# Kernel optimization log

Measured on AMD Instinct MI355X. Metric: run time of the kernel, lower is better.

The kernel has to match this reference:

```python
import jax, jax.numpy as jnp
import numpy as np

B = 30          # bandwidth
L = B           # degrees l = 0..L-1
NB = 2 * B      # spatial grid size per angle (beta/alpha/gamma)
MW = 2 * L - 1  # centered frequency index width, m in [-(L-1), L-1]
P = 6           # kernel grid points (n_alpha=6, n_beta=1)


def _wigner_d_all(betas, L):
    """Wigner-d matrices d^l_{m,n}(beta) via d^l(beta)=expm(-(beta/2)(J+ - J-)).
    Returns [len(betas), L, MW, MW], zero-padded for |m|,|n|>l."""
    betas = np.asarray(betas, dtype=np.float64)
    D = np.zeros((len(betas), L, MW, MW), dtype=np.float64)
    for l in range(L):
        dim = 2 * l + 1
        m = np.arange(-l, l)
        cp = np.sqrt(l * (l + 1) - m * (m + 1))  # <m+1|J+|m>
        A = np.zeros((dim, dim))
        A[np.arange(1, dim), np.arange(dim - 1)] = cp
        A = A - A.T  # J+ - J-, real antisymmetric
        lam, V = np.linalg.eigh(1j * A)  # Hermitian
        ph = np.exp(0.5j * betas[:, None] * lam[None, :])  # [nb, dim]
        dl = np.einsum('ab,jb,cb->jac', V, ph, V.conj()).real
        off = L - 1 - l
        D[:, l, off:off + dim, off:off + dim] = dl
    return D


def _s3_quadrature(b):
    """SOFT-grid quadrature weights over beta (lie_learn S3 formula, up to a constant)."""
    j = np.arange(2 * b)
    k = np.arange(b)[None, :]
    s = (np.sin(np.pi * (2 * j[:, None] + 1) * (2 * k + 1) / (4 * b)) / (2 * k + 1)).sum(axis=1)
    return (2.0 / b) * np.sin(np.pi * (2 * j + 1) / (4 * b)) * s


# ---- precomputed constants ----
_betas_sig = np.pi * (2 * np.arange(NB) + 1) / (4 * B)  # SOFT beta grid
_D_np = _wigner_d_all(_betas_sig, L)                    # [NB, L, MW, MW]
_alphas_k = np.linspace(0.0, 2.0 * np.pi, P, endpoint=False)
_Dk_np = _wigner_d_all(np.full(P, np.pi / 160.0), L)[:, :, :, L - 1]  # [P, L, MW], n=0 column
_idx_c = (np.arange(MW) - (L - 1)) % NB                 # centered m -> FFT bin
_nidx = np.arange(MW) - (L - 1)

D_SIG = jnp.asarray(_D_np, dtype=jnp.float32)
D0_SIG = jnp.asarray(_D_np[:, :, :, L - 1], dtype=jnp.float32)
D_KER = jnp.asarray(_Dk_np, dtype=jnp.float32)
W_QUAD = jnp.asarray(_s3_quadrature(B), dtype=jnp.float32)
FAC_L = jnp.asarray(2 * np.arange(L) + 1, dtype=jnp.float32)
E_KER = jnp.asarray(np.exp(-1j * _nidx[None, :] * _alphas_k[:, None]), dtype=jnp.complex64)


def s2_conv(x, wk):
    """FFT-based S2 convolution: S2 analysis -> spectral multiply -> SO(3) synthesis.
    x: [batch, f_in, NB(beta), NB(alpha)] real; wk: [f_in, f_out, P].
    Returns [batch, f_out, NB(beta), NB(alpha), NB(gamma)] real."""
    xf = jnp.fft.fft(x, axis=-1) * (2.0 * np.pi / NB)        # alpha -> m, complex64
    xfc = xf[..., _idx_c]                                     # centered m: [b,f,NB,MW]
    # S2 analysis: X^l_m = sum_beta w(beta) d^l_{m0}(beta) xhat(beta, m)
    X = jnp.einsum('j,jlm,bfjm->bflm', W_QUAD, D0_SIG, xfc)   # [b,f_in,L,MW]
    # kernel spectrum psi^l_n = sum_p wk_p d^l_{n0}(beta_p) e^{-i n alpha_p}
    psi = jnp.einsum('iop,pln,pn->ioln', wk.astype(jnp.complex64),
                     D_KER.astype(jnp.complex64), E_KER)      # [f_in,f_out,L,MW]
    # spectral mm: Z^l_{mn} = sum_{f_in} X^l_m conj(psi^l_n)
    Z = jnp.einsum('bilm,ioln->bolmn', X, jnp.conj(psi))      # [b,f_out,L,MW,MW]
    # SO(3) synthesis per beta: F(beta,m,n) = sum_l (2l+1) d^l_{mn}(beta) Z^l_{mn}
    F = jnp.einsum('l,jlmn,bolmn->bojmn', FAC_L, D_SIG, Z)    # [b,f_out,NB,MW,MW]
    G = jnp.zeros(F.shape[:3] + (NB, NB), dtype=F.dtype)
    G = G.at[..., _idx_c[:, None], _idx_c[None, :]].set(F)    # embed centered freqs
    return jnp.fft.ifft2(G, axes=(-2, -1)).real * float(NB * NB)


def so3_integrate_gamma(x):
    # matches the given so3_integrate: contracts ONLY the last (gamma) axis with w
    return jnp.einsum('...g,g->...', x, W_QUAD)


def setup_inputs() -> dict:
    key = jax.random.key(0)
    k1, k2, k3 = jax.random.split(key, 3)
    batch = 16
    x1 = jax.random.normal(k1, (batch, 2, NB, NB), dtype=jnp.float32)
    w_conv = jax.random.normal(k2, (2, 10, P), dtype=jnp.float32) / np.sqrt(2 * P)
    w_deconv = jax.random.normal(k3, (10, 2, P), dtype=jnp.float32) / np.sqrt(10 * P)
    return {"x1": x1, "w_conv": w_conv, "w_deconv": w_deconv}


def reference(x1, w_conv, w_deconv):
    x = s2_conv(x1, w_conv)        # encode: [b,10,60,60,60]
    x = so3_integrate_gamma(x)     # [b,10,60,60] (S2 signal)
    x = s2_conv(x, w_deconv)       # decode: [b,2,60,60,60]
    return so3_integrate_gamma(x)  # [b,2,60,60]
```

## Files before the change

kernel.cpp:

```cpp
#include <hip/hip_runtime.h>
#include <hip/hip_fp16.h>

#define NBG   60
#define LMAX  30
#define MWC   59
#define CTR   29
#define NPAIR 20
#define NT    11
#define NTP   12
#define NOFF  5
#define PI_F  3.14159265358979323846f

__device__ void wigner_colf(float beta, int mp, int mn, float scale,
                            float* out, int stride) {
  int a = mp - mn; if (a < 0) a = -a;
  int b = mp + mn; if (b < 0) b = -b;
  int lmin = (a + b) >> 1;
  for (int l = 0; l < LMAX; ++l) out[l * stride] = 0.0f;
  if (lmin >= LMAX) return;
  float sh, ch; sincosf(0.5f * beta, &sh, &ch);
  float x = ch * ch - sh * sh;
  float base = scale;
  for (int q = 0; q < a; ++q) base *= sh;
  for (int q = 0; q < b; ++q) base *= ch;
  if (mp >= mn && ((mp - mn) & 1)) base = -base;
  float K2 = 1.f;
  for (int q = 1; q <= a; ++q) K2 *= (float)(b + q) / (float)q;
  float Pm2 = 0.f, Pm1 = 1.f;
  out[lmin * stride] = base * sqrtf(K2);
  for (int s = 1; lmin + s < LMAX; ++s) {
    float Ps;
    if (s == 1) {
      Ps = (a + 1) + (a + b + 2) * 0.5f * (x - 1.f);
    } else {
      float t0 = 2.f * s + a + b;
      float c1 = 2.f * s * (s + a + b) * (t0 - 2.f);
      float c2 = (t0 - 1.f) * (t0 * (t0 - 2.f) * x + (float)(a * a - b * b));
      float c3 = 2.f * (s + a - 1.f) * (s + b - 1.f) * t0;
      Ps = (c2 * Pm1 - c3 * Pm2) / c1;
    }
    K2 *= ((float)s * (s + a + b)) / (((float)s + a) * ((float)s + b));
    out[(lmin + s) * stride] = base * sqrtf(K2) * Ps;
    Pm2 = Pm1; Pm1 = Ps;
  }
}

__device__ __forceinline__ float quad_w(int j) {
  float s = 0.f;
  for (int k = 0; k < 30; ++k) {
    int r = ((2 * j + 1) * (2 * k + 1)) % 240;
    s += sinf(2.f * PI_F * r / 240.f) / (float)(2 * k + 1);
  }
  return (2.f / 30.f) * sinf(PI_F * (2 * j + 1) / 120.f) * s;
}

__global__ __launch_bounds__(256)
void k1_prep(const float* __restrict__ x1,
             const float* __restrict__ wc, const float* __restrict__ wd,
             float2* __restrict__ scwF1, float2* __restrict__ scwF2,
             float* __restrict__ D0T, float* __restrict__ sgd,
             float2* __restrict__ xfT) {
  __shared__ __align__(16) char smem[13056];
  int u = blockIdx.x, t = threadIdx.x;
  if (u == 0) {
    float*  swq  = (float*)smem;
    float2* swqn = (float2*)(smem + 256);
    if (t < NBG) swq[t] = quad_w(t);
    __syncthreads();
    if (t < NT) {
      int n = t - NOFF;
      float re = 0.f, im = 0.f;
      for (int g = 0; g < NBG; ++g) {
        int k = ((n * g) % NBG + NBG) % NBG;
        float sn, cs; sincosf(2.f * PI_F * k / 60.f, &sn, &cs);
        re += swq[g] * cs; im += swq[g] * sn;
      }
      swqn[t] = make_float2(re, im);
    }
    __syncthreads();
    if (t < NT * NPAIR) {
      int nn = t / NPAIR, pair = t - nn * NPAIR, n = nn - NOFF;
      float re1 = 0, im1 = 0, re2 = 0, im2 = 0;
      for (int p = 0; p < 6; ++p) {
        int k = ((n * p) % 6 + 6) % 6;
        float sn, cs; sincosf(2.f * PI_F * k / 6.f, &sn, &cs);
        float a1 = wc[pair * 6 + p], a2 = wd[pair * 6 + p];
        re1 += a1 * cs; im1 += a1 * sn;
        re2 += a2 * cs; im2 += a2 * sn;
      }
      float2 w = swqn[nn];
      scwF1[t] = make_float2(w.x * re1 - w.y * im1, w.x * im1 + w.y * re1);
      scwF2[t] = make_float2(PI_F * (w.x * re2 - w.y * im2),
                             PI_F * (w.x * im2 + w.y * re2));
    }
  } else if (u < 60) {
    int M = u - 1;
    if (t < NBG) {
      float wqj = quad_w(t);
      wigner_colf(PI_F * (2 * t + 1) / 120.f, M - CTR, 0, wqj,
                  D0T + (size_t)M * LMAX * NBG + t, NBG);
    }
  } else if (u < 300) {
    float* buf  = (float*)smem;
    float* dkwL = (float*)(smem + 11520);
    int s = u - 60, j = s >> 2, c = s & 3;
    int M0 = c * 8, nM = (c < 3) ? 8 : 6;
    if (t < nM * NT) {
      int Mi = t / NT, nn = t - Mi * NT;
      wigner_colf(PI_F * (2 * j + 1) / 120.f, M0 + Mi - CTR, nn - NOFF, 1.f,
                  &buf[Mi * 360 + nn], NTP);
    } else if (t >= 128 && t < 128 + NT) {
      int nn = t - 128;
      wigner_colf(PI_F / 160.f, nn - NOFF, 0, 1.f, dkwL + nn, NTP);
      for (int l = 0; l < LMAX; ++l) dkwL[l * NTP + nn] *= (float)(2 * l + 1);
    }
    __syncthreads();
    size_t base = (size_t)(j * 30 + M0) * 360;
    for (int q = t; q < nM * 360; q += 256) {
      int r = q % 360, nn = r % NTP;
      sgd[base + q] = (nn < NT) ? buf[q] * dkwL[r] : 0.f;
    }
  } else {
    float*  xr  = (float*)smem;
    float*  twc = (float*)(smem + 1920);
    float*  tws = (float*)(smem + 2160);
    float2* xo  = (float2*)(smem + 2400);
    int s = u - 300, j = s >> 2, qh = s & 3;
    for (int q = t; q < 8 * NBG; q += 256) {
      int bl = q / NBG, a = q - bl * NBG;
      xr[bl * NBG + a] = x1[((size_t)(qh * 8 + bl) * NBG + j) * NBG + a];
    }
    if (t < NBG) {
      float sn, cs; sincosf(-2.f * PI_F * t / 60.f, &sn, &cs);
      twc[t] = cs; tws[t] = sn;
    }
    __syncthreads();
    for (int q = t; q < 8 * MWC; q += 256) {
      int bl = q / MWC, M = q - bl * MWC, mm = M - CTR;
      const float* xp = xr + bl * NBG;
      float re = 0.f, im = 0.f; int k = 0;
      for (int a = 0; a < NBG; ++a) {
        re += xp[a] * twc[k]; im += xp[a] * tws[k];
        k += mm; if (k >= NBG) k -= NBG; if (k < 0) k += NBG;
      }
      const float sc = 2.f * PI_F / 60.f;
      xo[M * 9 + bl] = make_float2(re * sc, im * sc);
    }
    __syncthreads();
    for (int q = t; q < MWC * 8; q += 256) {
      int M = q / 8, bl = q - M * 8;
      xfT[((size_t)M * NBG + j) * 32 + qh * 8 + bl] = xo[M * 9 + bl];
    }
  }
}

__global__ __launch_bounds__(256)
void k_ana1(const float2* __restrict__ xfT, const float* __restrict__ D0T,
            float2* __restrict__ X21) {
  __shared__ float2 sxf[NBG][16];
  __shared__ float  sD[8][NBG];
  int bi = blockIdx.x;
  int M = bi >> 3, lq = (bi >> 1) & 3, wh = bi & 1;
  int t = threadIdx.x;
  for (int q = t; q < NBG * 16; q += 256) {
    int jj = q >> 4, b = q & 15;
    sxf[jj][b] = xfT[((size_t)M * NBG + jj) * 32 + b * 2 + wh];
  }
  for (int q = t; q < 8 * NBG; q += 256) {
    int ll = q / NBG, jj = q - ll * NBG, l = lq * 8 + ll;
    sD[ll][jj] = (l < LMAX) ? D0T[((size_t)M * LMAX + l) * NBG + jj] : 0.f;
  }
  __syncthreads();
  if (t < 128) {
    int ll = t >> 4, b = t & 15;
    int l = lq * 8 + ll;
    if (l < LMAX) {
      float re = 0.f, im = 0.f;
#pragma unroll 6
      for (int jj = 0; jj < NBG; ++jj) {
        float d = sD[ll][jj];
        float2 v = sxf[jj][b];
        re += d * v.x; im += d * v.y;
      }
      X21[(size_t)M * LMAX * 32 + l * 32 + wh * 16 + b] = make_float2(re, im);
    }
  }
}

__global__ __launch_bounds__(256)
void k_core1(const float2* __restrict__ X2, const float* __restrict__ sgd,
             const float2* __restrict__ scwF, __half2* __restrict__ Th) {
  __shared__ float  sg[2][LMAX][NTP];
  __shared__ float2 scw[NT * NPAIR];
  __shared__ float2 sC[2][LMAX][NPAIR];
  int t = threadIdx.x;
  int j = blockIdx.x / 30, mg = blockIdx.x - 30 * j;
  int Mbase = mg * 2;
  for (int q = t; q < NT * NPAIR; q += 256) scw[q] = scwF[q];
  for (int q = t; q < 2 * LMAX * NTP; q += 256) {
    int Mi = q / (LMAX * NTP), r = q - Mi * LMAX * NTP;
    int l = r / NTP, nn = r - l * NTP;
    int M = Mbase + Mi;
    float v = 0.f;
    if (M < MWC && nn < NT) {
      if (M < 30) {
        v = sgd[(size_t)(j * 30 + M) * 360 + r];
      } else {
        v = sgd[(size_t)(j * 30 + 58 - M) * 360 + l * NTP + (10 - nn)];
        if (!(M & 1)) v = -v;
      }
    }
    ((float*)sg)[q] = v;
  }
  __syncthreads();
  for (int q = t; q < 2 * LMAX * NPAIR; q += 256) {
    int Mi = q / (LMAX * NPAIR), r = q - Mi * LMAX * NPAIR;
    int l = r / NPAIR, pair = r - l * NPAIR;
    float cre = 0.f, cim = 0.f;
#pragma unroll
    for (int nn = 0; nn < NT; ++nn) {
      float g = sg[Mi][l][nn];
      float2 c = scw[nn * NPAIR + pair];
      cre += g * c.x; cim += g * c.y;
    }
    ((float2*)sC)[q] = make_float2(cre, cim);
  }
  __syncthreads();
  for (int q = t; q < 2 * 160; q += 256) {
    int Mi = q / 160, u = q - Mi * 160;
    int M = Mbase + Mi;
    if (M >= MWC) continue;
    int bb = u / 10, o = u - 10 * bb;
    float tre = 0.f, tim = 0.f;
#pragma unroll 6
    for (int l = 0; l < LMAX; ++l) {
#pragma unroll
      for (int i = 0; i < 2; ++i) {
        float2 xv = X2[((size_t)M * LMAX + l) * 32 + i * 16 + bb];
        float2 cv = sC[Mi][l][i * 10 + o];
        tre += xv.x * cv.x - xv.y * cv.y;
        tim += xv.x * cv.y + xv.y * cv.x;
      }
    }
    Th[((size_t)j * MWC + M) * 160 + u] = __floats2half2_rn(tre, tim);
  }
}

__global__ __launch_bounds__(256)
void k_ana2(const __half2* __restrict__ T1, const float* __restrict__ D0T,
            float2* __restrict__ X22) {
  __shared__ float2 sxf[NBG][10];
  __shared__ float  sD[LMAX][NBG];
  int M = blockIdx.x >> 4, c = blockIdx.x & 15;
  int u0 = c * 10, t = threadIdx.x;
  for (int q = t; q < NBG * 10; q += 256) {
    int jj = q / 10, w = q - jj * 10;
    float2 v1 = __half22float2(T1[((size_t)jj * MWC + M) * 160 + u0 + w]);
    float2 v2 = __half22float2(T1[((size_t)jj * MWC + (58 - M)) * 160 + u0 + w]);
    sxf[jj][w] = make_float2(v1.x + v2.x, v1.y - v2.y);
  }
  for (int q = t; q < LMAX * NBG; q += 256) ((float*)sD)[q] = D0T[(size_t)M * LMAX * NBG + q];
  __syncthreads();
  for (int q = t; q < LMAX * 10; q += 256) {
    int l = q / 10, w = q - l * 10;
    float re = 0.f, im = 0.f;
#pragma unroll 6
    for (int jj = 0; jj < NBG; ++jj) {
      float d = sD[l][jj];
      float2 v = sxf[jj][w];
      re += d * v.x; im += d * v.y;
    }
    X22[((size_t)M * LMAX + l) * 160 + w * 16 + c] = make_float2(re, im);
  }
}

__global__ __launch_bounds__(256)
void k_core2(const float2* __restrict__ X2, const float* __restrict__ sgd,
             const float2* __restrict__ scwF, float2* __restrict__ Tf) {
  __shared__ float  sg[2][LMAX][NTP];
  __shared__ float2 scw[NT * NPAIR];
  __shared__ float2 sC[2][LMAX][NPAIR];
  __shared__ float2 sRed[256];
  int t = threadIdx.x;
  int j = blockIdx.x / 30, mg = blockIdx.x - 30 * j;
  int Mbase = mg * 2;
  for (int q = t; q < NT * NPAIR; q += 256) scw[q] = scwF[q];
  for (int q = t; q < 2 * LMAX * NTP; q += 256) {
    int Mi = q / (LMAX * NTP), r = q - Mi * LMAX * NTP;
    int l = r / NTP, nn = r - l * NTP;
    int M = Mbase + Mi;
    float v = 0.f;
    if (M < MWC && nn < NT) {
      if (M < 30) {
        v = sgd[(size_t)(j * 30 + M) * 360 + r];
      } else {
        v = sgd[(size_t)(j * 30 + 58 - M) * 360 + l * NTP + (10 - nn)];
        if (!(M & 1)) v = -v;
      }
    }
    ((float*)sg)[q] = v;
  }
  __syncthreads();
  for (int q = t; q < 2 * LMAX * NPAIR; q += 256) {
    int Mi = q / (LMAX * NPAIR), r = q - Mi * LMAX * NPAIR;
    int l = r / NPAIR, pair = r - l * NPAIR;
    float cre = 0.f, cim = 0.f;
#pragma unroll
    for (int nn = 0; nn < NT; ++nn) {
      float g = sg[Mi][l][nn];
      float2 c = scw[nn * NPAIR + pair];
      cre += g * c.x; cim += g * c.y;
    }
    ((float2*)sC)[q] = make_float2(cre, cim);
  }
  __syncthreads();
  int sub = t >> 6, idx = t & 63;
  int Mi = idx >> 5, u = idx & 31;
  int M = Mbase + Mi;
  int bb = u >> 1, o = u & 1;
  float tre = 0.f, tim = 0.f;
  if (M < MWC) {
    for (int l = sub; l < LMAX; l += 4) {
#pragma unroll
      for (int i = 0; i < 10; ++i) {
        float2 xv = X2[((size_t)M * LMAX + l) * 160 + i * 16 + bb];
        float2 cv = sC[Mi][l][i * 2 + o];
        tre += xv.x * cv.x - xv.y * cv.y;
        tim += xv.x * cv.y + xv.y * cv.x;
      }
    }
  }
  sRed[t] = make_float2(tre, tim);
  __syncthreads();
  if (t < 64 && M < MWC) {
    float2 a0 = sRed[t], a1 = sRed[t + 64], a2 = sRed[t + 128], a3 = sRed[t + 192];
    Tf[((size_t)j * MWC + M) * 32 + u] =
        make_float2(a0.x + a1.x + a2.x + a3.x, a0.y + a1.y + a2.y + a3.y);
  }
}

__global__ __launch_bounds__(256)
void k_synth2(const float2* __restrict__ T2, float* __restrict__ out) {
  __shared__ float2 sT[MWC][8];
  __shared__ float twc[NBG], tws[NBG];
  int j = blockIdx.x >> 2, uq = blockIdx.x & 3;
  int u0 = uq * 8, t = threadIdx.x;
  for (int q = t; q < MWC * 8; q += 256) {
    int M = q >> 3, uu = q & 7;
    sT[M][uu] = T2[((size_t)j * MWC + M) * 32 + u0 + uu];
  }
  if (t < NBG) {
    float s, c; sincosf(2.f * PI_F * t / 60.f, &s, &c);
    twc[t] = c; tws[t] = s;
  }
  __syncthreads();
  for (int q = t; q < 8 * NBG; q += 256) {
    int uu = q / NBG, a = q - uu * NBG;
    int k = (31 * a) % NBG;
    float acc = 0.f;
#pragma unroll 4
    for (int M = 0; M < MWC; ++M) {
      float2 v = sT[M][uu];
      acc += v.x * twc[k] - v.y * tws[k];
      k += a; if (k >= NBG) k -= NBG;
    }
    out[((size_t)(u0 + uu) * NBG + j) * NBG + a] = acc;
  }
}

extern "C" void kernel_launch(void* const* d_in, const int* in_sizes, int n_in,
                              void* d_out, int out_size, void* d_ws, size_t ws_size,
                              hipStream_t stream) {
  const float* x1 = (const float*)d_in[0];
  const float* wc = (const float*)d_in[1];
  const float* wd = (const float*)d_in[2];
  float* out = (float*)d_out;
  char* ws = (char*)d_ws;

  float2*  scwF1 = (float2*) (ws + 0);
  float2*  scwF2 = (float2*) (ws + 2048);
  float*   D0T   = (float*)  (ws + 4096);
  float*   sgd   = (float*)  (ws + 430080);
  char*    R1    = ws + 3022592;
  char*    R2    = ws + 5288192;
  float2*  X21   = (float2*) (ws + 7553792);
  float2*  xfT   = (float2*) R1;
  float2*  X22   = (float2*) R1;
  __half2* T1    = (__half2*)R2;
  float2*  T2    = (float2*) R2;

  k1_prep <<<540,  256, 0, stream>>>(x1, wc, wd, scwF1, scwF2, D0T, sgd, xfT);
  k_ana1  <<<472,  256, 0, stream>>>(xfT, D0T, X21);
  k_core1 <<<1800, 256, 0, stream>>>(X21, sgd, scwF1, T1);
  k_ana2  <<<944,  256, 0, stream>>>(T1, D0T, X22);
  k_core2 <<<1800, 256, 0, stream>>>(X22, sgd, scwF2, T2);
  k_synth2<<<240,  256, 0, stream>>>(T2, out);
}
```

Measured before the change: 91.42 us.

## Fuse alpha-DFT and first beta analysis into prep kernel, drop k_ana1

```diff
diff --git a/kernel.cpp b/kernel.cpp
--- a/kernel.cpp
+++ b/kernel.cpp
@@ -59,8 +59,8 @@
              const float* __restrict__ wc, const float* __restrict__ wd,
              float2* __restrict__ scwF1, float2* __restrict__ scwF2,
              float* __restrict__ D0T, float* __restrict__ sgd,
-             float2* __restrict__ xfT) {
-  __shared__ __align__(16) char smem[13056];
+             float2* __restrict__ X21) {
+  __shared__ __align__(16) char smem[15360];
   int u = blockIdx.x, t = threadIdx.x;
   if (u == 0) {
     float*  swq  = (float*)smem;
@@ -121,68 +121,49 @@
       sgd[base + q] = (nn < NT) ? buf[q] * dkwL[r] : 0.f;
     }
   } else {
-    float*  xr  = (float*)smem;
-    float*  twc = (float*)(smem + 1920);
-    float*  tws = (float*)(smem + 2160);
-    float2* xo  = (float2*)(smem + 2400);
-    int s = u - 300, j = s >> 2, qh = s & 3;
-    for (int q = t; q < 8 * NBG; q += 256) {
-      int bl = q / NBG, a = q - bl * NBG;
-      xr[bl * NBG + a] = x1[((size_t)(qh * 8 + bl) * NBG + j) * NBG + a];
-    }
+    float*  twc = (float*)smem;
+    float*  tws = (float*)(smem + 240);
+    float2* sxf = (float2*)(smem + 480);
+    float*  sDf = (float*)(smem + 8160);
+    int bi = u - 300;
+    int M = bi >> 3, lq = (bi >> 1) & 3, wh = bi & 1;
+    int mm = M - CTR;
     if (t < NBG) {
       float sn, cs; sincosf(-2.f * PI_F * t / 60.f, &sn, &cs);
       twc[t] = cs; tws[t] = sn;
     }
-    __syncthreads();
-    for (int q = t; q < 8 * MWC; q += 256) {
-      int bl = q / MWC, M = q - bl * MWC, mm = M - CTR;
-      const float* xp = xr + bl * NBG;
+    if (t >= 64 && t < 64 + NBG) {
+      int j = t - 64;
+      float wqj = quad_w(j);
+      wigner_colf(PI_F * (2 * j + 1) / 120.f, mm, 0, wqj, sDf + j, NBG);
+    }
+    __syncthreads();
+    for (int q = t; q < NBG * 16; q += 256) {
+      int j = q >> 4, b = q & 15;
+      const float* xp = x1 + ((size_t)(2 * b + wh) * NBG + j) * NBG;
       float re = 0.f, im = 0.f; int k = 0;
+#pragma unroll
       for (int a = 0; a < NBG; ++a) {
         re += xp[a] * twc[k]; im += xp[a] * tws[k];
         k += mm; if (k >= NBG) k -= NBG; if (k < 0) k += NBG;
       }
       const float sc = 2.f * PI_F / 60.f;
-      xo[M * 9 + bl] = make_float2(re * sc, im * sc);
-    }
-    __syncthreads();
-    for (int q = t; q < MWC * 8; q += 256) {
-      int M = q / 8, bl = q - M * 8;
-      xfT[((size_t)M * NBG + j) * 32 + qh * 8 + bl] = xo[M * 9 + bl];
-    }
-  }
-}
-
-__global__ __launch_bounds__(256)
-void k_ana1(const float2* __restrict__ xfT, const float* __restrict__ D0T,
-            float2* __restrict__ X21) {
-  __shared__ float2 sxf[NBG][16];
-  __shared__ float  sD[8][NBG];
-  int bi = blockIdx.x;
-  int M = bi >> 3, lq = (bi >> 1) & 3, wh = bi & 1;
-  int t = threadIdx.x;
-  for (int q = t; q < NBG * 16; q += 256) {
-    int jj = q >> 4, b = q & 15;
-    sxf[jj][b] = xfT[((size_t)M * NBG + jj) * 32 + b * 2 + wh];
-  }
-  for (int q = t; q < 8 * NBG; q += 256) {
-    int ll = q / NBG, jj = q - ll * NBG, l = lq * 8 + ll;
-    sD[ll][jj] = (l < LMAX) ? D0T[((size_t)M * LMAX + l) * NBG + jj] : 0.f;
-  }
-  __syncthreads();
-  if (t < 128) {
-    int ll = t >> 4, b = t & 15;
-    int l = lq * 8 + ll;
-    if (l < LMAX) {
-      float re = 0.f, im = 0.f;
+      sxf[q] = make_float2(re * sc, im * sc);
+    }
+    __syncthreads();
+    if (t < 128) {
+      int ll = t >> 4, b = t & 15;
+      int l = lq * 8 + ll;
+      if (l < LMAX) {
+        float re = 0.f, im = 0.f;
 #pragma unroll 6
-      for (int jj = 0; jj < NBG; ++jj) {
-        float d = sD[ll][jj];
-        float2 v = sxf[jj][b];
-        re += d * v.x; im += d * v.y;
-      }
-      X21[(size_t)M * LMAX * 32 + l * 32 + wh * 16 + b] = make_float2(re, im);
+        for (int jj = 0; jj < NBG; ++jj) {
+          float d = sDf[l * NBG + jj];
+          float2 v = sxf[jj * 16 + b];
+          re += d * v.x; im += d * v.y;
+        }
+        X21[(size_t)M * LMAX * 32 + l * 32 + wh * 16 + b] = make_float2(re, im);
+      }
     }
   }
 }
@@ -384,13 +365,11 @@
   char*    R1    = ws + 3022592;
   char*    R2    = ws + 5288192;
   float2*  X21   = (float2*) (ws + 7553792);
-  float2*  xfT   = (float2*) R1;
   float2*  X22   = (float2*) R1;
   __half2* T1    = (__half2*)R2;
   float2*  T2    = (float2*) R2;
 
-  k1_prep <<<540,  256, 0, stream>>>(x1, wc, wd, scwF1, scwF2, D0T, sgd, xfT);
-  k_ana1  <<<472,  256, 0, stream>>>(xfT, D0T, X21);
+  k1_prep <<<772,  256, 0, stream>>>(x1, wc, wd, scwF1, scwF2, D0T, sgd, X21);
   k_core1 <<<1800, 256, 0, stream>>>(X21, sgd, scwF1, T1);
   k_ana2  <<<944,  256, 0, stream>>>(T1, D0T, X22);
   k_core2 <<<1800, 256, 0, stream>>>(X22, sgd, scwF2, T2);
```

Result: slower. 96.89 us (+6.0%).
